# Kernel tuning notes

Hardware: AMD Instinct MI355X
Metric: run time of the kernel (lower is better)

## Reference

```python
import jax, jax.numpy as jnp
import numpy as np

B, P, Q, N, D, K_HEADCHUNK = 16, 12, 12, 2048, 64, 8


def setup_inputs() -> dict:
    key = jax.random.key(0)
    ks = jax.random.split(key, 8)
    mkw = lambda k, sh: (jax.random.normal(k, sh, jnp.float32) * 0.05)
    return {
        "x": jax.random.normal(ks[0], (B, P, N, D), jnp.float32),
        "STE_P": jax.random.normal(ks[1], (B, P, N, D), jnp.float32),
        "STE_Q": jax.random.normal(ks[2], (B, Q, N, D), jnp.float32),
        # shared input projection (applied to query, key AND value in the original)
        "W_ff": mkw(ks[3], (D, D)), "b_ff": jnp.zeros((D,), jnp.float32),
        # two-layer output FFN
        "W1": mkw(ks[4], (D, D)), "b1": jnp.zeros((D,), jnp.float32),
        "W2": mkw(ks[5], (D, D)), "b2": jnp.zeros((D,), jnp.float32),
        "K": K_HEADCHUNK,
    }


def reference(x, STE_P, STE_Q, W_ff, b_ff, W1, b1, W2, b2, K):
    # Faithful to torch source: split(..., K, dim=-1) makes chunks of SIZE K,
    # i.e. h = D // K heads (h == self.d), each with head_dim K. Scale is d**0.5.
    Dm = x.shape[-1]
    h = Dm // K                      # number of heads (= self.d in torch code)
    scale = 1.0 / np.sqrt(float(h))  # attention /= self.d ** 0.5

    q = STE_Q @ W_ff + b_ff          # [B, Q, N, D]
    k = STE_P @ W_ff + b_ff          # [B, P, N, D]
    v = x @ W_ff + b_ff              # [B, P, N, D]

    Bb, Tq, Nn = q.shape[0], q.shape[1], q.shape[2]
    Tp = k.shape[1]
    qh = q.reshape(Bb, Tq, Nn, h, K)
    kh = k.reshape(Bb, Tp, Nn, h, K)
    vh = v.reshape(Bb, Tp, Nn, h, K)

    scores = jnp.einsum('bqnhk,bpnhk->bhnqp', qh, kh) * scale  # [B,h,N,Q,P]
    attn = jax.nn.softmax(scores, axis=-1)
    out = jnp.einsum('bhnqp,bpnhk->bqnhk', attn, vh).reshape(Bb, Tq, Nn, Dm)

    hid = jax.nn.relu(out @ W1 + b1)
    return hid @ W2 + b2             # [B, Q, N, D]
```

## Files before the change

kernel.cpp:

```cpp
#include <hip/hip_runtime.h>
#include <hip/hip_bf16.h>


typedef __attribute__((ext_vector_type(8))) short bf16x8;
typedef __attribute__((ext_vector_type(4))) float f32x4;

constexpr int Bb = 16, Ss = 12, Nn = 2048, Dd = 64;
constexpr float EXPK = 0.51011687f;
constexpr int KOFS = 12288, VOFS = 24576, LDSZ = 36864;

#define MFMA16(A, B, C) __builtin_amdgcn_mfma_f32_16x16x32_bf16((A), (B), (C), 0, 0, 0)

__device__ __forceinline__ short f2bf(float f) {
    __hip_bfloat16 h = __float2bfloat16(f);
    short s; __builtin_memcpy(&s, &h, 2); return s;
}
__device__ __forceinline__ float bitf(unsigned u) {
    float f; __builtin_memcpy(&f, &u, 4); return f;
}
__device__ __forceinline__ float bf2f(unsigned short v) {
    return bitf(((unsigned)v) << 16);
}
__device__ __forceinline__ unsigned cvtpk(float lo, float hi) {
    unsigned r;
    asm("v_cvt_pk_bf16_f32 %0, %1, %2" : "=v"(r) : "v"(lo), "v"(hi));
    return r;
}
__device__ __forceinline__ void lds_fence() {
    asm volatile("s_waitcnt lgkmcnt(0)" ::: "memory");
    __builtin_amdgcn_sched_barrier(0);
}
__device__ __forceinline__ int qkOfs(int t, int s, int n, int d) {
    return t * KOFS + s * 1024 + n * 128 + ((2 * d) ^ (((s & 7) ^ (n & 7)) << 4));
}
__device__ __forceinline__ int tOfs(int w, int ni, int row, int d) {
    return w * 6144 + ni * 3072 + row * 128 + ((2 * d) ^ ((row & 7) << 4));
}

__global__ void prep_w(const float* __restrict__ Wff, const float* __restrict__ W1,
                       const float* __restrict__ W2, unsigned short* __restrict__ wt) {
    int idx = blockIdx.x * 256 + threadIdx.x;
    if (idx >= 3 * 4096) return;
    int m = idx >> 12, rc = idx & 4095, r = rc >> 6, c = rc & 63;
    const float* W = (m == 0) ? Wff : (m == 1) ? W1 : W2;
    unsigned short u; short s = f2bf(W[c * 64 + r]);
    __builtin_memcpy(&u, &s, 2);
    wt[idx] = u;
}

__global__ __launch_bounds__(256, 4)
void ta_mfma8(const float* __restrict__ x,
              const float* __restrict__ steP,
              const float* __restrict__ steQ,
              const float* __restrict__ bff, const float* __restrict__ b1,
              const float* __restrict__ b2,
              const unsigned short* __restrict__ wt,
              float* __restrict__ out)
{
    alignas(16) __shared__ char smem[LDSZ];

    const int tid = threadIdx.x;
    const int w   = tid >> 6;
    const int l   = tid & 63;
    const int l15 = l & 15;
    const int l4  = l >> 4;
    const int b   = blockIdx.y;
    const int n0  = blockIdx.x * 8;

    bf16x8 wf[4][2];
    float bfv[4];
    #pragma unroll
    for (int nt = 0; nt < 4; ++nt) {
        bfv[nt] = bff[nt * 16 + l15];
        #pragma unroll
        for (int kc = 0; kc < 2; ++kc)
            wf[nt][kc] = *(const bf16x8*)(wt + (nt * 16 + l15) * 64 + kc * 32 + l4 * 8);
    }

    const int sA = l15 >> 3, nA = l15 & 7;
    for (int job = w; job < 18; job += 4) {
        const int t = job / 6, s0 = (job % 6) * 2;
        const float* base = (t == 0) ? steQ : (t == 1) ? steP : x;
        const float* rp = base + ((size_t)(b * Ss + s0 + sA) * Nn + n0 + nA) * Dd + l4 * 8;

        bf16x8 a[2];
        #pragma unroll
        for (int kc = 0; kc < 2; ++kc) {
            float4 p0 = *(const float4*)(rp + kc * 32);
            float4 p1 = *(const float4*)(rp + kc * 32 + 4);
            union { unsigned u[4]; bf16x8 v; } cv;
            cv.u[0] = cvtpk(p0.x, p0.y); cv.u[1] = cvtpk(p0.z, p0.w);
            cv.u[2] = cvtpk(p1.x, p1.y); cv.u[3] = cvtpk(p1.z, p1.w);
            a[kc] = cv.v;
        }
        #pragma unroll
        for (int nt = 0; nt < 4; ++nt) {
            f32x4 acc = { bfv[nt], bfv[nt], bfv[nt], bfv[nt] };
            acc = MFMA16(a[0], wf[nt][0], acc);
            acc = MFMA16(a[1], wf[nt][1], acc);
            const int d = nt * 16 + l15;
            #pragma unroll
            for (int q = 0; q < 4; ++q) {
                const int r = l4 * 4 + q, s = s0 + (r >> 3), nn = r & 7;
                *(short*)(smem + qkOfs(t, s, nn, d)) = f2bf(acc[q]);
            }
        }
    }
    __syncthreads();

    float vv[2][12];
    #pragma unroll
    for (int ni = 0; ni < 2; ++ni)
        #pragma unroll
        for (int s = 0; s < 12; ++s)
            vv[ni][s] = bf2f(*(const unsigned short*)(smem + qkOfs(2, s, w * 2 + ni, l)));

    unsigned pw[2][8][2];
    #pragma unroll
    for (int h = 0; h < 8; ++h) {
        #pragma unroll
        for (int ni = 0; ni < 2; ++ni) {
            const int n = w * 2 + ni;
            union { unsigned u[4]; bf16x8 v; } akk;
            akk.v = *(const bf16x8*)(smem + qkOfs(1, l15, n, h * 8));
            bf16x8 aq = *(const bf16x8*)(smem + qkOfs(0, l15, n, h * 8));
            if (l4 != 0) { akk.u[0] = 0; akk.u[1] = 0; akk.u[2] = 0; akk.u[3] = 0; }
            f32x4 c = { 0.f, 0.f, 0.f, 0.f };
            c = MFMA16(akk.v, aq, c);
            float e[4];
            #pragma unroll
            for (int i = 0; i < 4; ++i) {
                float v = __builtin_amdgcn_exp2f(c[i] * EXPK);
                e[i] = (l4 == 3) ? 0.f : v;
            }
            float ssum = (e[0] + e[1]) + (e[2] + e[3]);
            ssum += __shfl_xor(ssum, 16);
            ssum += __shfl_xor(ssum, 32);
            float inv;
            asm("v_rcp_f32 %0, %1" : "=v"(inv) : "v"(ssum));
            pw[ni][h][0] = cvtpk(e[0] * inv, e[1] * inv);
            pw[ni][h][1] = cvtpk(e[2] * inv, e[3] * inv);
        }
    }
    __syncthreads();

    #pragma unroll
    for (int ni = 0; ni < 2; ++ni) {
        const int pb = w * 6144 + ni * 3072;
        if (l15 < 12 && l4 < 3) {
            #pragma unroll
            for (int h = 0; h < 8; ++h) {
                uint2 u; u.x = pw[ni][h][0]; u.y = pw[ni][h][1];
                *(uint2*)(smem + pb + l15 * 256 + ((h * 32) ^ ((l15 & 7) << 5)) + l4 * 8) = u;
            }
        }
    }
    lds_fence();

    float oacc[2][12];
    const int hslot = (l >> 3) * 32;
    #pragma unroll
    for (int q = 0; q < 12; ++q) {
        #pragma unroll
        for (int ni = 0; ni < 2; ++ni) {
            const char* qp = smem + w * 6144 + ni * 3072 + q * 256 + (hslot ^ ((q & 7) << 5));
            uint4 pa = *(const uint4*)(qp);
            uint2 pbx = *(const uint2*)(qp + 16);
            const unsigned wds[6] = { pa.x, pa.y, pa.z, pa.w, pbx.x, pbx.y };
            float a = 0.f;
            #pragma unroll
            for (int p2 = 0; p2 < 6; ++p2) {
                a = fmaf(bitf(wds[p2] << 16),         vv[ni][2 * p2],     a);
                a = fmaf(bitf(wds[p2] & 0xFFFF0000u), vv[ni][2 * p2 + 1], a);
            }
            oacc[ni][q] = a;
        }
    }
    lds_fence();

    #pragma unroll
    for (int ni = 0; ni < 2; ++ni)
        #pragma unroll
        for (int q = 0; q < 12; ++q)
            *(short*)(smem + tOfs(w, ni, q, l)) = f2bf(oacc[ni][q]);
    lds_fence();

    {
        bf16x8 w1f[4][2];
        float b1v[4];
        #pragma unroll
        for (int nt = 0; nt < 4; ++nt) {
            b1v[nt] = b1[nt * 16 + l15];
            #pragma unroll
            for (int kc = 0; kc < 2; ++kc)
                w1f[nt][kc] = *(const bf16x8*)(wt + 4096 + (nt * 16 + l15) * 64 + kc * 32 + l4 * 8);
        }
        #pragma unroll
        for (int ni = 0; ni < 2; ++ni) {
            bf16x8 a[2];
            #pragma unroll
            for (int kc = 0; kc < 2; ++kc)
                a[kc] = *(const bf16x8*)(smem + tOfs(w, ni, l15, kc * 32 + l4 * 8));
            #pragma unroll
            for (int nt = 0; nt < 4; ++nt) {
                f32x4 acc = { b1v[nt], b1v[nt], b1v[nt], b1v[nt] };
                acc = MFMA16(a[0], w1f[nt][0], acc);
                acc = MFMA16(a[1], w1f[nt][1], acc);
                #pragma unroll
                for (int reg = 0; reg < 4; ++reg) {
                    const int rt = l4 * 4 + reg;
                    if (rt < 12)
                        *(short*)(smem + tOfs(w, ni, rt, nt * 16 + l15)) =
                            f2bf(fmaxf(acc[reg], 0.f));
                }
            }
        }
    }
    lds_fence();
    {
        bf16x8 w2f[4][2];
        float b2v[4];
        #pragma unroll
        for (int nt = 0; nt < 4; ++nt) {
            b2v[nt] = b2[nt * 16 + l15];
            #pragma unroll
            for (int kc = 0; kc < 2; ++kc)
                w2f[nt][kc] = *(const bf16x8*)(wt + 8192 + (nt * 16 + l15) * 64 + kc * 32 + l4 * 8);
        }
        #pragma unroll
        for (int ni = 0; ni < 2; ++ni) {
            bf16x8 a[2];
            #pragma unroll
            for (int kc = 0; kc < 2; ++kc)
                a[kc] = *(const bf16x8*)(smem + tOfs(w, ni, l15, kc * 32 + l4 * 8));
            #pragma unroll
            for (int nt = 0; nt < 4; ++nt) {
                f32x4 acc = { b2v[nt], b2v[nt], b2v[nt], b2v[nt] };
                acc = MFMA16(a[0], w2f[nt][0], acc);
                acc = MFMA16(a[1], w2f[nt][1], acc);
                #pragma unroll
                for (int reg = 0; reg < 4; ++reg) {
                    const int q = l4 * 4 + reg;
                    if (q < 12)
                        out[((size_t)(b * Ss + q) * Nn + n0 + w * 2 + ni) * Dd + nt * 16 + l15] = acc[reg];
                }
            }
        }
    }
}

extern "C" void kernel_launch(void* const* d_in, const int* in_sizes, int n_in,
                              void* d_out, int out_size, void* d_ws, size_t ws_size,
                              hipStream_t stream) {
    const float* x    = (const float*)d_in[0];
    const float* steP = (const float*)d_in[1];
    const float* steQ = (const float*)d_in[2];
    const float* Wff  = (const float*)d_in[3];
    const float* bff  = (const float*)d_in[4];
    const float* W1   = (const float*)d_in[5];
    const float* b1   = (const float*)d_in[6];
    const float* W2   = (const float*)d_in[7];
    const float* b2   = (const float*)d_in[8];
    float* out = (float*)d_out;
    unsigned short* wtp = (unsigned short*)d_ws;

    prep_w<<<48, 256, 0, stream>>>(Wff, W1, W2, wtp);
    dim3 grid(Nn / 8, Bb);
    ta_mfma8<<<grid, 256, 0, stream>>>(x, steP, steQ, bff, b1, b2, wtp, out);
}
```

Before: 127.6 us.

## Shrink LDS footprint by reusing Q/K buffers for V and per-wave scratch

Reduces shared memory from 36 KB to 24 KB. V is now projected only after the score/softmax phase and written into the freed Q slot. The probability and FFN scratch is packed into the K slot, with each wave's two nodes processed serially. The intent is to let more blocks fit per CU and so improve occupancy and latency hiding for this memory-bound kernel. The cost is an extra barrier, serialized V loads that no longer overlap with the QK work, and more LDS fences.

```diff
diff --git a/kernel.cpp b/kernel.cpp
--- a/kernel.cpp
+++ b/kernel.cpp
@@ -7,7 +7,7 @@
 
 constexpr int Bb = 16, Ss = 12, Nn = 2048, Dd = 64;
 constexpr float EXPK = 0.51011687f;
-constexpr int KOFS = 12288, VOFS = 24576, LDSZ = 36864;
+constexpr int KOFS = 12288, LDSZ = 24576;
 
 #define MFMA16(A, B, C) __builtin_amdgcn_mfma_f32_16x16x32_bf16((A), (B), (C), 0, 0, 0)
 
@@ -33,8 +33,8 @@
 __device__ __forceinline__ int qkOfs(int t, int s, int n, int d) {
     return t * KOFS + s * 1024 + n * 128 + ((2 * d) ^ (((s & 7) ^ (n & 7)) << 4));
 }
-__device__ __forceinline__ int tOfs(int w, int ni, int row, int d) {
-    return w * 6144 + ni * 3072 + row * 128 + ((2 * d) ^ ((row & 7) << 4));
+__device__ __forceinline__ int tRow(int row, int d) {
+    return row * 128 + ((2 * d) ^ ((row & 7) << 4));
 }
 
 __global__ void prep_w(const float* __restrict__ Wff, const float* __restrict__ W1,
@@ -49,13 +49,13 @@
 }
 
 __global__ __launch_bounds__(256, 4)
-void ta_mfma8(const float* __restrict__ x,
-              const float* __restrict__ steP,
-              const float* __restrict__ steQ,
-              const float* __restrict__ bff, const float* __restrict__ b1,
-              const float* __restrict__ b2,
-              const unsigned short* __restrict__ wt,
-              float* __restrict__ out)
+void ta_mfma13(const float* __restrict__ x,
+               const float* __restrict__ steP,
+               const float* __restrict__ steQ,
+               const float* __restrict__ bff, const float* __restrict__ b1,
+               const float* __restrict__ b2,
+               const unsigned short* __restrict__ wt,
+               float* __restrict__ out)
 {
     alignas(16) __shared__ char smem[LDSZ];
 
@@ -78,11 +78,8 @@
     }
 
     const int sA = l15 >> 3, nA = l15 & 7;
-    for (int job = w; job < 18; job += 4) {
-        const int t = job / 6, s0 = (job % 6) * 2;
-        const float* base = (t == 0) ? steQ : (t == 1) ? steP : x;
+    auto do_job = [&](const float* base, int tSlot, int s0) {
         const float* rp = base + ((size_t)(b * Ss + s0 + sA) * Nn + n0 + nA) * Dd + l4 * 8;
-
         bf16x8 a[2];
         #pragma unroll
         for (int kc = 0; kc < 2; ++kc) {
@@ -102,19 +99,18 @@
             #pragma unroll
             for (int q = 0; q < 4; ++q) {
                 const int r = l4 * 4 + q, s = s0 + (r >> 3), nn = r & 7;
-                *(short*)(smem + qkOfs(t, s, nn, d)) = f2bf(acc[q]);
-            }
-        }
+                *(short*)(smem + qkOfs(tSlot, s, nn, d)) = f2bf(acc[q]);
+            }
+        }
+    };
+
+    for (int job = w; job < 12; job += 4) {
+        const int t = job / 6, s0 = (job % 6) * 2;
+        do_job((t == 0) ? steQ : steP, t, s0);
     }
     __syncthreads();
 
-    float vv[2][12];
-    #pragma unroll
-    for (int ni = 0; ni < 2; ++ni)
-        #pragma unroll
-        for (int s = 0; s < 12; ++s)
-            vv[ni][s] = bf2f(*(const unsigned short*)(smem + qkOfs(2, s, w * 2 + ni, l)));
-
+    const int sE = (l15 < 12) ? l15 : 11;
     unsigned pw[2][8][2];
     #pragma unroll
     for (int h = 0; h < 8; ++h) {
@@ -122,8 +118,8 @@
         for (int ni = 0; ni < 2; ++ni) {
             const int n = w * 2 + ni;
             union { unsigned u[4]; bf16x8 v; } akk;
-            akk.v = *(const bf16x8*)(smem + qkOfs(1, l15, n, h * 8));
-            bf16x8 aq = *(const bf16x8*)(smem + qkOfs(0, l15, n, h * 8));
+            akk.v = *(const bf16x8*)(smem + qkOfs(1, sE, n, h * 8));
+            bf16x8 aq = *(const bf16x8*)(smem + qkOfs(0, sE, n, h * 8));
             if (l4 != 0) { akk.u[0] = 0; akk.u[1] = 0; akk.u[2] = 0; akk.u[3] = 0; }
             f32x4 c = { 0.f, 0.f, 0.f, 0.f };
             c = MFMA16(akk.v, aq, c);
@@ -144,26 +140,34 @@
     }
     __syncthreads();
 
+    for (int job = w; job < 6; job += 4)
+        do_job(x, 0, job * 2);
+    __syncthreads();
+
+    float vv[2][12];
+    #pragma unroll
+    for (int ni = 0; ni < 2; ++ni)
+        #pragma unroll
+        for (int s = 0; s < 12; ++s)
+            vv[ni][s] = bf2f(*(const unsigned short*)(smem + qkOfs(0, s, w * 2 + ni, l)));
+    lds_fence();
+
+    char* const pbBase = smem + KOFS + w * 3072;
+    const int hslot = (l >> 3) * 32;
+    float oacc[2][12];
     #pragma unroll
     for (int ni = 0; ni < 2; ++ni) {
-        const int pb = w * 6144 + ni * 3072;
         if (l15 < 12 && l4 < 3) {
             #pragma unroll
             for (int h = 0; h < 8; ++h) {
                 uint2 u; u.x = pw[ni][h][0]; u.y = pw[ni][h][1];
-                *(uint2*)(smem + pb + l15 * 256 + ((h * 32) ^ ((l15 & 7) << 5)) + l4 * 8) = u;
-            }
-        }
-    }
-    lds_fence();
-
-    float oacc[2][12];
-    const int hslot = (l >> 3) * 32;
-    #pragma unroll
-    for (int q = 0; q < 12; ++q) {
-        #pragma unroll
-        for (int ni = 0; ni < 2; ++ni) {
-            const char* qp = smem + w * 6144 + ni * 3072 + q * 256 + (hslot ^ ((q & 7) << 5));
+                *(uint2*)(pbBase + l15 * 256 + ((h * 32) ^ ((l15 & 7) << 5)) + l4 * 8) = u;
+            }
+        }
+        lds_fence();
+        #pragma unroll
+        for (int q = 0; q < 12; ++q) {
+            const char* qp = pbBase + q * 256 + (hslot ^ ((q & 7) << 5));
             uint4 pa = *(const uint4*)(qp);
             uint2 pbx = *(const uint2*)(qp + 16);
             const unsigned wds[6] = { pa.x, pa.y, pa.z, pa.w, pbx.x, pbx.y };
@@ -175,15 +179,17 @@
             }
             oacc[ni][q] = a;
         }
-    }
+        lds_fence();
+    }
+
+    #pragma unroll
+    for (int ni = 0; ni < 2; ++ni)
+        #pragma unroll
+        for (int q = 0; q < 12; ++q)
+            *(short*)(pbBase + ni * 1536 + tRow(q, l)) = f2bf(oacc[ni][q]);
     lds_fence();
 
-    #pragma unroll
-    for (int ni = 0; ni < 2; ++ni)
-        #pragma unroll
-        for (int q = 0; q < 12; ++q)
-            *(short*)(smem + tOfs(w, ni, q, l)) = f2bf(oacc[ni][q]);
-    lds_fence();
+    const int l15c = (l15 < 12) ? l15 : 0;
 
     {
         bf16x8 w1f[4][2];
@@ -200,7 +206,7 @@
             bf16x8 a[2];
             #pragma unroll
             for (int kc = 0; kc < 2; ++kc)
-                a[kc] = *(const bf16x8*)(smem + tOfs(w, ni, l15, kc * 32 + l4 * 8));
+                a[kc] = *(const bf16x8*)(pbBase + ni * 1536 + tRow(l15c, kc * 32 + l4 * 8));
             #pragma unroll
             for (int nt = 0; nt < 4; ++nt) {
                 f32x4 acc = { b1v[nt], b1v[nt], b1v[nt], b1v[nt] };
@@ -210,7 +216,7 @@
                 for (int reg = 0; reg < 4; ++reg) {
                     const int rt = l4 * 4 + reg;
                     if (rt < 12)
-                        *(short*)(smem + tOfs(w, ni, rt, nt * 16 + l15)) =
+                        *(short*)(pbBase + ni * 1536 + tRow(rt, nt * 16 + l15)) =
                             f2bf(fmaxf(acc[reg], 0.f));
                 }
             }
@@ -232,7 +238,7 @@
             bf16x8 a[2];
             #pragma unroll
             for (int kc = 0; kc < 2; ++kc)
-                a[kc] = *(const bf16x8*)(smem + tOfs(w, ni, l15, kc * 32 + l4 * 8));
+                a[kc] = *(const bf16x8*)(pbBase + ni * 1536 + tRow(l15c, kc * 32 + l4 * 8));
             #pragma unroll
             for (int nt = 0; nt < 4; ++nt) {
                 f32x4 acc = { b2v[nt], b2v[nt], b2v[nt], b2v[nt] };
@@ -266,5 +272,5 @@
 
     prep_w<<<48, 256, 0, stream>>>(Wff, W1, W2, wtp);
     dim3 grid(Nn / 8, Bb);
-    ta_mfma8<<<grid, 256, 0, stream>>>(x, steP, steQ, bff, b1, b2, wtp, out);
-}
+    ta_mfma13<<<grid, 256, 0, stream>>>(x, steP, steQ, bff, b1, b2, wtp, out);
+}
```

Result: slower. 152.5 us (+19.5%).

## Stage projection inputs through LDS via direct global-to-LDS loads

Applied to the files above, without the earlier changes.

Input rows for the Q/K/V projection are now fetched with global_load_lds into a per-wave swizzled LDS staging buffer and then read back from LDS, instead of being loaded straight into registers. The attention output and FFN intermediates now reuse the V region of LDS rather than a separate area. The aim is to make the global reads more efficient and coalesced. In exchange, LDS grows to 52 KB, launch bounds drop to 3 blocks per SM, and each job waits on vmcnt(0) with no overlap across jobs.

```diff
diff --git a/kernel.cpp b/kernel.cpp
--- a/kernel.cpp
+++ b/kernel.cpp
@@ -7,7 +7,7 @@
 
 constexpr int Bb = 16, Ss = 12, Nn = 2048, Dd = 64;
 constexpr float EXPK = 0.51011687f;
-constexpr int KOFS = 12288, VOFS = 24576, LDSZ = 36864;
+constexpr int KOFS = 12288, VOFS = 24576, STG = 36864, LDSZ = 53248;
 
 #define MFMA16(A, B, C) __builtin_amdgcn_mfma_f32_16x16x32_bf16((A), (B), (C), 0, 0, 0)
 
@@ -30,11 +30,15 @@
     asm volatile("s_waitcnt lgkmcnt(0)" ::: "memory");
     __builtin_amdgcn_sched_barrier(0);
 }
+__device__ __forceinline__ void vm_fence0() {
+    asm volatile("s_waitcnt vmcnt(0)" ::: "memory");
+    __builtin_amdgcn_sched_barrier(0);
+}
 __device__ __forceinline__ int qkOfs(int t, int s, int n, int d) {
     return t * KOFS + s * 1024 + n * 128 + ((2 * d) ^ (((s & 7) ^ (n & 7)) << 4));
 }
-__device__ __forceinline__ int tOfs(int w, int ni, int row, int d) {
-    return w * 6144 + ni * 3072 + row * 128 + ((2 * d) ^ ((row & 7) << 4));
+__device__ __forceinline__ int vtOfs(int slot, int row, int d) {
+    return VOFS + slot * 1536 + row * 128 + ((2 * d) ^ ((row & 7) << 4));
 }
 
 __global__ void prep_w(const float* __restrict__ Wff, const float* __restrict__ W1,
@@ -48,14 +52,14 @@
     wt[idx] = u;
 }
 
-__global__ __launch_bounds__(256, 4)
-void ta_mfma8(const float* __restrict__ x,
-              const float* __restrict__ steP,
-              const float* __restrict__ steQ,
-              const float* __restrict__ bff, const float* __restrict__ b1,
-              const float* __restrict__ b2,
-              const unsigned short* __restrict__ wt,
-              float* __restrict__ out)
+__global__ __launch_bounds__(256, 3)
+void ta_mfma14(const float* __restrict__ x,
+               const float* __restrict__ steP,
+               const float* __restrict__ steQ,
+               const float* __restrict__ bff, const float* __restrict__ b1,
+               const float* __restrict__ b2,
+               const unsigned short* __restrict__ wt,
+               float* __restrict__ out)
 {
     alignas(16) __shared__ char smem[LDSZ];
 
@@ -77,20 +81,38 @@
             wf[nt][kc] = *(const bf16x8*)(wt + (nt * 16 + l15) * 64 + kc * 32 + l4 * 8);
     }
 
-    const int sA = l15 >> 3, nA = l15 & 7;
-    for (int job = w; job < 18; job += 4) {
+    char* const sbuf = smem + STG + w * 4096;
+    const int nj = (w < 2) ? 5 : 4;
+
+    for (int jj = 0; jj < nj; ++jj) {
+        const int job = w + jj * 4;
         const int t = job / 6, s0 = (job % 6) * 2;
         const float* base = (t == 0) ? steQ : (t == 1) ? steP : x;
-        const float* rp = base + ((size_t)(b * Ss + s0 + sA) * Nn + n0 + nA) * Dd + l4 * 8;
-
+
+        lds_fence();
+        #pragma unroll
+        for (int i = 0; i < 4; ++i) {
+            const int r = i * 4 + l4;
+            const char* src = (const char*)base
+                + ((size_t)(b * Ss + s0 + (r >> 3)) * Nn + n0 + (r & 7)) * 256
+                + ((l15 * 16) ^ ((r & 7) << 5));
+            __builtin_amdgcn_global_load_lds(
+                (const __attribute__((address_space(1))) unsigned*)(const void*)src,
+                (__attribute__((address_space(3))) unsigned*)(void*)(sbuf + i * 1024),
+                16, 0, 0);
+        }
+        vm_fence0();
+
+        const int rsw = (l15 & 7) << 5;
         bf16x8 a[2];
         #pragma unroll
         for (int kc = 0; kc < 2; ++kc) {
-            float4 p0 = *(const float4*)(rp + kc * 32);
-            float4 p1 = *(const float4*)(rp + kc * 32 + 4);
+            const int d0 = kc * 128 + l4 * 32;
+            f32x4 p0 = *(const f32x4*)(sbuf + l15 * 256 + (d0 ^ rsw));
+            f32x4 p1 = *(const f32x4*)(sbuf + l15 * 256 + ((d0 + 16) ^ rsw));
             union { unsigned u[4]; bf16x8 v; } cv;
-            cv.u[0] = cvtpk(p0.x, p0.y); cv.u[1] = cvtpk(p0.z, p0.w);
-            cv.u[2] = cvtpk(p1.x, p1.y); cv.u[3] = cvtpk(p1.z, p1.w);
+            cv.u[0] = cvtpk(p0[0], p0[1]); cv.u[1] = cvtpk(p0[2], p0[3]);
+            cv.u[2] = cvtpk(p1[0], p1[1]); cv.u[3] = cvtpk(p1[2], p1[3]);
             a[kc] = cv.v;
         }
         #pragma unroll
@@ -176,14 +198,15 @@
             oacc[ni][q] = a;
         }
     }
+
+    #pragma unroll
+    for (int ni = 0; ni < 2; ++ni)
+        #pragma unroll
+        for (int q = 0; q < 12; ++q)
+            *(short*)(smem + vtOfs(w * 2 + ni, q, l)) = f2bf(oacc[ni][q]);
     lds_fence();
 
-    #pragma unroll
-    for (int ni = 0; ni < 2; ++ni)
-        #pragma unroll
-        for (int q = 0; q < 12; ++q)
-            *(short*)(smem + tOfs(w, ni, q, l)) = f2bf(oacc[ni][q]);
-    lds_fence();
+    const int l15c = (l15 < 12) ? l15 : 0;
 
     {
         bf16x8 w1f[4][2];
@@ -197,10 +220,11 @@
         }
         #pragma unroll
         for (int ni = 0; ni < 2; ++ni) {
+            const int slot = w * 2 + ni;
             bf16x8 a[2];
             #pragma unroll
             for (int kc = 0; kc < 2; ++kc)
-                a[kc] = *(const bf16x8*)(smem + tOfs(w, ni, l15, kc * 32 + l4 * 8));
+                a[kc] = *(const bf16x8*)(smem + vtOfs(slot, l15c, kc * 32 + l4 * 8));
             #pragma unroll
             for (int nt = 0; nt < 4; ++nt) {
                 f32x4 acc = { b1v[nt], b1v[nt], b1v[nt], b1v[nt] };
@@ -210,7 +234,7 @@
                 for (int reg = 0; reg < 4; ++reg) {
                     const int rt = l4 * 4 + reg;
                     if (rt < 12)
-                        *(short*)(smem + tOfs(w, ni, rt, nt * 16 + l15)) =
+                        *(short*)(smem + vtOfs(slot, rt, nt * 16 + l15)) =
                             f2bf(fmaxf(acc[reg], 0.f));
                 }
             }
@@ -229,10 +253,11 @@
         }
         #pragma unroll
         for (int ni = 0; ni < 2; ++ni) {
+            const int slot = w * 2 + ni;
             bf16x8 a[2];
             #pragma unroll
             for (int kc = 0; kc < 2; ++kc)
-                a[kc] = *(const bf16x8*)(smem + tOfs(w, ni, l15, kc * 32 + l4 * 8));
+                a[kc] = *(const bf16x8*)(smem + vtOfs(slot, l15c, kc * 32 + l4 * 8));
             #pragma unroll
             for (int nt = 0; nt < 4; ++nt) {
                 f32x4 acc = { b2v[nt], b2v[nt], b2v[nt], b2v[nt] };
@@ -242,7 +267,7 @@
                 for (int reg = 0; reg < 4; ++reg) {
                     const int q = l4 * 4 + reg;
                     if (q < 12)
-                        out[((size_t)(b * Ss + q) * Nn + n0 + w * 2 + ni) * Dd + nt * 16 + l15] = acc[reg];
+                        out[((size_t)(b * Ss + q) * Nn + n0 + slot) * Dd + nt * 16 + l15] = acc[reg];
                 }
             }
         }
@@ -266,5 +291,5 @@
 
     prep_w<<<48, 256, 0, stream>>>(Wff, W1, W2, wtp);
     dim3 grid(Nn / 8, Bb);
-    ta_mfma8<<<grid, 256, 0, stream>>>(x, steP, steQ, bff, b1, b2, wtp, out);
-}
+    ta_mfma14<<<grid, 256, 0, stream>>>(x, steP, steQ, bff, b1, b2, wtp, out);
+}
```

New measurement: 127.9 us. Within noise of the previous version (+0.3%).
